# Optimization experiments

Measured on AMD Instinct MI355X. Metric: run time of the kernel, lower is better.

Reference implementation:

```python
import jax, jax.numpy as jnp
import numpy as np

N_CELLS, C_N, K, D_N = 128, 256, 16, 64
G, HS, HM, HMOD, HEADS = 8, 128, 128, 64, 4


def setup_inputs() -> dict:
    key = jax.random.key(0)
    ks = list(jax.random.split(key, 12))
    rng = np.random.default_rng(0)
    # top-K neighbors per neuron within each cell, self excluded, sorted (as in __init__)
    scores = rng.random((N_CELLS, C_N, C_N), dtype=np.float32)
    scores[:, np.arange(C_N), np.arange(C_N)] = -np.inf
    topk = np.argpartition(-scores, K, axis=-1)[..., :K]
    conn_idx = jnp.asarray(np.sort(topk, axis=-1).astype(np.int32))
    cell_to_group = jnp.asarray((np.arange(N_CELLS) % G).astype(np.int32))

    def nrm(k, shape, scale):
        return jax.random.normal(k, shape, dtype=jnp.float32) * scale

    inp = {
        'h': nrm(ks[0], (N_CELLS, C_N, D_N), 1.0),
        'neuron_id': nrm(ks[1], (N_CELLS, C_N, D_N), 0.02),
        'neuron_key': nrm(ks[2], (N_CELLS, C_N, D_N), 0.02),
        'state_w1': nrm(ks[3], (HS, 2 * D_N), (2.0 / (2 * D_N)) ** 0.5),
        'state_b1': jnp.zeros((HS,), jnp.float32),
        'state_gs1': jnp.ones((G, HS), jnp.float32),
        'state_gb1': jnp.zeros((G, HS), jnp.float32),
        'state_w2': nrm(ks[4], (D_N, HS), 0.1 * (2.0 / HS) ** 0.5),
        'state_b2': jnp.zeros((D_N,), jnp.float32),
        'state_gs2': jnp.ones((G, D_N), jnp.float32),
        'state_gb2': jnp.zeros((G, D_N), jnp.float32),
        'msg_w1': nrm(ks[5], (HM, 2 * D_N), (2.0 / (2 * D_N)) ** 0.5),
        'msg_b1': jnp.zeros((HM,), jnp.float32),
        'msg_gs1': jnp.ones((G, HM), jnp.float32),
        'msg_gb1': jnp.zeros((G, HM), jnp.float32),
        'msg_w2': nrm(ks[6], (D_N, HM), 0.1 * (2.0 / HM) ** 0.5),
        'msg_b2': jnp.zeros((D_N,), jnp.float32),
        'msg_gs2': jnp.ones((G, D_N), jnp.float32),
        'msg_gb2': jnp.zeros((G, D_N), jnp.float32),
        'mod_w1': nrm(ks[7], (N_CELLS, D_N, HMOD), (2.0 / D_N) ** 0.5),
        'mod_b1': jnp.zeros((N_CELLS, HMOD), jnp.float32),
        'mod_w2': nrm(ks[8], (N_CELLS, HMOD, D_N), 0.01 * (2.0 / HMOD) ** 0.5),
        'mod_b2': jnp.zeros((N_CELLS, D_N), jnp.float32),
        'conn_idx': conn_idx,
        'cell_to_group': cell_to_group,
    }
    return inp


def reference(h, neuron_id, neuron_key,
              state_w1, state_b1, state_gs1, state_gb1,
              state_w2, state_b2, state_gs2, state_gb2,
              msg_w1, msg_b1, msg_gs1, msg_gb1,
              msg_w2, msg_b2, msg_gs2, msg_gb2,
              mod_w1, mod_b1, mod_w2, mod_b2,
              conn_idx, cell_to_group):
    g = cell_to_group  # [N]
    dh = D_N // HEADS
    gather = jax.vmap(lambda per_cell, idx: per_cell[idx])  # [C,D],[C,K] -> [C,K,D]

    nbr = gather(h, conn_idx)          # [N,C,K,D] neighbor states
    kid = gather(neuron_id, conn_idx)  # [N,C,K,D] neighbor identity vectors

    # multi-head attention weights over the K neighbors
    q = neuron_key.reshape(N_CELLS, C_N, HEADS, dh)
    kk = kid.reshape(N_CELLS, C_N, K, HEADS, dh)
    logits = jnp.einsum('nchd,nckhd->nckh', q, kk) / (dh ** 0.5)
    attn = jax.nn.softmax(logits, axis=2)  # softmax over K

    # per-edge message MLP with per-group gain/bias
    x = jnp.concatenate([nbr, jnp.broadcast_to(h[:, :, None, :], nbr.shape)], axis=-1)  # [N,C,K,2D]
    m1 = jax.nn.gelu(jnp.einsum('nckf,hf->nckh', x, msg_w1) + msg_b1)
    m1 = m1 * msg_gs1[g][:, None, None, :] + msg_gb1[g][:, None, None, :]
    m2 = jnp.einsum('nckh,dh->nckd', m1, msg_w2) + msg_b2
    m2 = m2 * msg_gs2[g][:, None, None, :] + msg_gb2[g][:, None, None, :]

    # attention-weighted aggregation over neighbors
    m2h = m2.reshape(N_CELLS, C_N, K, HEADS, dh)
    agg = jnp.einsum('nckh,nckhd->nchd', attn, m2h).reshape(N_CELLS, C_N, D_N)

    # state-update MLP with per-group gain/bias
    s_in = jnp.concatenate([h, agg], axis=-1)  # [N,C,2D]
    s1 = jax.nn.gelu(jnp.einsum('ncf,hf->nch', s_in, state_w1) + state_b1)
    s1 = s1 * state_gs1[g][:, None, :] + state_gb1[g][:, None, :]
    delta = jnp.einsum('nch,dh->ncd', s1, state_w2) + state_b2
    delta = delta * state_gs2[g][:, None, :] + state_gb2[g][:, None, :]

    # per-cell batched modulation MLP (mod_w1/mod_w2) gating the update
    pooled = h.mean(axis=1)  # [N,D]
    mh = jnp.tanh(jnp.einsum('nd,ndh->nh', pooled, mod_w1) + mod_b1)
    gate = jnp.tanh(jnp.einsum('nh,nho->no', mh, mod_w2) + mod_b2)  # [N,D]

    return h + gate[:, None, :] * delta
```

## Files before the change

### kernel.cpp

```cpp
#include <hip/hip_runtime.h>
#include <hip/hip_bf16.h>

#define N_CELLS 128
#define C_N     256
#define K_NB    16
#define D_N     64
#define G_N     8
#define HS      128
#define HM      128
#define HMOD    64

typedef __bf16 bf16x8 __attribute__((ext_vector_type(8)));
typedef float  f32x4v __attribute__((ext_vector_type(4)));
typedef _Float16 half2_t __attribute__((ext_vector_type(2)));


__device__ __forceinline__ unsigned cvtpk(float lo, float hi) {
    __hip_bfloat162 t = __float22bfloat162_rn(float2{lo, hi});
    return *reinterpret_cast<unsigned*>(&t);
}

__device__ __forceinline__ unsigned short f2bf(float f) {
    return (unsigned short)(cvtpk(f, 0.f) & 0xffffu);
}

__device__ __forceinline__ float bflo(unsigned u) { return __uint_as_float(u << 16); }
__device__ __forceinline__ float bfhi(unsigned u) { return __uint_as_float(u & 0xffff0000u); }

__device__ __forceinline__ half2_t pkrtz(float lo, float hi) {
    return __builtin_bit_cast(half2_t, __builtin_amdgcn_cvt_pkrtz(lo, hi));
}

__device__ __forceinline__ half2_t h2(unsigned u) {
    return __builtin_bit_cast(half2_t, u);
}

__device__ __forceinline__ f32x4v mfma16(uint4 a, uint4 b, f32x4v c) {
    return __builtin_amdgcn_mfma_f32_16x16x32_bf16(
        __builtin_bit_cast(bf16x8, a), __builtin_bit_cast(bf16x8, b), c, 0, 0, 0);
}

__device__ __forceinline__ float gelu_f(float x) {
    float x2 = x * x;
    float u  = x * fmaf(x2, 0.044715f, 1.0f);
    float e  = __expf(1.5957691216057308f * u);
    float r  = __builtin_amdgcn_rcpf(e + 1.0f);
    return x - x * r;
}

__device__ __forceinline__ float sgelu(float x) {
    float e = __expf(-1.702f * x);
    float r = __builtin_amdgcn_rcpf(e + 1.0f);
    return x * r;
}

__device__ __forceinline__ float tanh_fast(float z) {
    float e = __expf(2.0f * z);
    return 1.0f - 2.0f / (e + 1.0f);
}

__device__ __forceinline__ uint4 packf8(const float* p) {
    float4 a = *(const float4*)p, b = *(const float4*)(p + 4);
    return make_uint4(cvtpk(a.x, a.y), cvtpk(a.z, a.w), cvtpk(b.x, b.y), cvtpk(b.z, b.w));
}

__device__ __forceinline__ void load_w2_folded(
    const float* __restrict__ w2, const float* __restrict__ gs1,
    const float* __restrict__ gb1, const float* __restrict__ gs2,
    const float* __restrict__ b2, const float* __restrict__ gb2,
    int g, int lrow, int lgrp, uint4 wf[4][4], float c2[4])
{
    #pragma unroll
    for (int nb2 = 0; nb2 < 4; ++nb2) {
        int d = nb2 * 16 + lrow;
        float gs2d = gs2[g * 64 + d];
        float cgb = 0.0f;
        #pragma unroll
        for (int kf = 0; kf < 4; ++kf) {
            int k0 = kf * 32 + lgrp * 8;
            const float* wp = w2 + d * 128 + k0;
            float4 wa = *(const float4*)wp, wb = *(const float4*)(wp + 4);
            const float* gp = gs1 + g * 128 + k0;
            float4 ga = *(const float4*)gp, gbv = *(const float4*)(gp + 4);
            const float* bp = gb1 + g * 128 + k0;
            float4 ba = *(const float4*)bp, bbv = *(const float4*)(bp + 4);
            cgb += wa.x*ba.x + wa.y*ba.y + wa.z*ba.z + wa.w*ba.w
                 + wb.x*bbv.x + wb.y*bbv.y + wb.z*bbv.z + wb.w*bbv.w;
            wf[nb2][kf] = make_uint4(
                cvtpk(wa.x*ga.x*gs2d,  wa.y*ga.y*gs2d),
                cvtpk(wa.z*ga.z*gs2d,  wa.w*ga.w*gs2d),
                cvtpk(wb.x*gbv.x*gs2d, wb.y*gbv.y*gs2d),
                cvtpk(wb.z*gbv.z*gs2d, wb.w*gbv.w*gs2d));
        }
        cgb += __shfl_xor(cgb, 16);
        cgb += __shfl_xor(cgb, 32);
        c2[nb2] = fmaf(gs2d, cgb + b2[d], gb2[g * 64 + d]);
    }
}


__global__ __launch_bounds__(512, 2) void prep_kernel(
    const float* __restrict__ h, const float* __restrict__ neuron_id,
    const float* __restrict__ neuron_key,
    const float* __restrict__ msg_w1, const float* __restrict__ msg_b1,
    const float* __restrict__ mod_w1, const float* __restrict__ mod_b1,
    const float* __restrict__ mod_w2, const float* __restrict__ mod_b2,
    const int* __restrict__ conn_idx,
    unsigned short* __restrict__ yws, unsigned short* __restrict__ bews,
    unsigned* __restrict__ att2, float* __restrict__ gatep)
{
    __shared__ __align__(16) unsigned short shmem[8][16 * 256];
    int tid = threadIdx.x, bid = blockIdx.x;
    int wave = tid >> 6, lane = tid & 63;
    int lrow = lane & 15, lgrp = lane >> 4;

    if (bid < 256) {
        int n = bid >> 1;
        int c0 = (bid & 1) * 128 + wave * 16;
        unsigned short* ybuf = shmem[wave];

        uint4 bf[2];
        {
            const float* hp = h + ((size_t)n * C_N + (c0 + lrow)) * 64;
            bf[0] = packf8(hp + lgrp * 8);
            bf[1] = packf8(hp + 32 + lgrp * 8);
        }
        for (int nbM = 0; nbM < 16; ++nbM) {
            int o = nbM * 16 + lrow;
            uint4 af[2];
            #pragma unroll
            for (int kf = 0; kf < 2; ++kf) {
                int k = kf * 32 + lgrp * 8;
                const float* wp = (o < 128) ? (msg_w1 + (size_t)o * 128 + k)
                                            : (msg_w1 + (size_t)(o - 128) * 128 + 64 + k);
                af[kf] = packf8(wp);
            }
            f32x4v acc = {0.f, 0.f, 0.f, 0.f};
            acc = mfma16(af[0], bf[0], acc);
            acc = mfma16(af[1], bf[1], acc);
            float4 addv = {0.f, 0.f, 0.f, 0.f};
            if (nbM >= 8) addv = *(const float4*)(msg_b1 + (nbM - 8) * 16 + lgrp * 4);
            uint2 pk = make_uint2(cvtpk(acc[0] + addv.x, acc[1] + addv.y),
                                  cvtpk(acc[2] + addv.z, acc[3] + addv.w));
            int byte = lrow * 512 + ((nbM * 32 + lgrp * 8) ^ ((lrow & 7) << 4));
            *reinterpret_cast<uint2*>(reinterpret_cast<char*>(ybuf) + byte) = pk;
        }
        #pragma unroll
        for (int pass = 0; pass < 8; ++pass) {
            int idx = pass * 64 + lane;
            int row = idx >> 5, col = idx & 31;
            int byte = row * 512 + ((col * 16) ^ ((row & 7) << 4));
            uint4 v = *reinterpret_cast<const uint4*>(
                reinterpret_cast<const char*>(ybuf) + byte);
            size_t rb = (((size_t)n * C_N + c0 + row) * 128) * 2;
            if (col < 16)
                *reinterpret_cast<uint4*>(reinterpret_cast<char*>(yws) + rb + col * 16) = v;
            else
                *reinterpret_cast<uint4*>(reinterpret_cast<char*>(bews) + rb + (col - 16) * 16) = v;
        }
    } else if (bid < 512) {
        int t = lgrp;
        int base = (bid - 256) * 128 + wave * 16;
        for (int i = 0; i < 16; ++i) {
            int gidx = base + i;
            int jv = conn_idx[(size_t)gidx * 16 + lrow];
            const float* kp = neuron_id + ((size_t)(gidx & ~255) + jv) * 64 + t * 16;
            const float* qp = neuron_key + (size_t)gidx * 64 + t * 16;
            float4 k0 = *(const float4*)kp,       k1 = *(const float4*)(kp + 4),
                   k2 = *(const float4*)(kp + 8), k3 = *(const float4*)(kp + 12);
            float4 q0 = *(const float4*)qp,       q1 = *(const float4*)(qp + 4),
                   q2 = *(const float4*)(qp + 8), q3 = *(const float4*)(qp + 12);
            float dt = k0.x*q0.x + k0.y*q0.y + k0.z*q0.z + k0.w*q0.w
                     + k1.x*q1.x + k1.y*q1.y + k1.z*q1.z + k1.w*q1.w
                     + k2.x*q2.x + k2.y*q2.y + k2.z*q2.z + k2.w*q2.w
                     + k3.x*q3.x + k3.y*q3.y + k3.z*q3.z + k3.w*q3.w;
            float lg = dt * 0.25f;
            float mx = lg;
            mx = fmaxf(mx, __shfl_xor(mx, 1));
            mx = fmaxf(mx, __shfl_xor(mx, 2));
            mx = fmaxf(mx, __shfl_xor(mx, 4));
            mx = fmaxf(mx, __shfl_xor(mx, 8));
            float ex = __expf(lg - mx);
            float sm = ex;
            sm += __shfl_xor(sm, 1);
            sm += __shfl_xor(sm, 2);
            sm += __shfl_xor(sm, 4);
            sm += __shfl_xor(sm, 8);
            float av = ex * __builtin_amdgcn_rcpf(sm);
            float avn = __shfl_down(av, 1);
            if ((lrow & 1) == 0) {
                att2[(size_t)gidx * 32 + (lrow >> 1) * 4 + t] =
                    __builtin_bit_cast(unsigned, __builtin_amdgcn_cvt_pkrtz(av, avn));
            }
        }
    } else {
        int n = bid - 512;
        float* red   = reinterpret_cast<float*>(shmem);
        float* pooled = red + 8 * 64;
        float* mh     = pooled + 64;
        int d = lane, part = wave;
        const float* hn = h + (size_t)n * C_N * 64;
        float acc = 0.0f;
        #pragma unroll 4
        for (int i = 0; i < 32; ++i) acc += hn[(part * 32 + i) * 64 + d];
        red[part * 64 + d] = acc;
        __syncthreads();
        if (tid < 64) {
            float s = 0.0f;
            #pragma unroll
            for (int p = 0; p < 8; ++p) s += red[p * 64 + d];
            pooled[d] = s * (1.0f / 256.0f);
        }
        __syncthreads();
        if (tid < 64) {
            float a1 = mod_b1[n * HMOD + d];
            for (int q = 0; q < 64; ++q)
                a1 = fmaf(pooled[q], mod_w1[((size_t)n * 64 + q) * HMOD + d], a1);
            mh[d] = tanh_fast(a1);
        }
        __syncthreads();
        if (tid < 64) {
            float a2 = mod_b2[n * 64 + d];
            for (int q = 0; q < HMOD; ++q)
                a2 = fmaf(mh[q], mod_w2[((size_t)n * HMOD + q) * 64 + d], a2);
            gatep[n * 64 + d] = tanh_fast(a2);
        }
    }
}


__global__ __launch_bounds__(1024, 4) void edge_kernel(
    const unsigned short* __restrict__ yws, const unsigned short* __restrict__ bews,
    const unsigned* __restrict__ att2, const int* __restrict__ conn_idx,
    const float* __restrict__ msg_w2, const float* __restrict__ msg_gs1,
    const float* __restrict__ msg_gb1, const float* __restrict__ msg_gs2,
    const float* __restrict__ msg_b2, const float* __restrict__ msg_gb2,
    const int* __restrict__ cell_to_group,
    unsigned short* __restrict__ aggws)
{
    __shared__ __align__(16) uint4 w2l[16 * 64];
    __shared__ float mb2cl[64];
    __shared__ __align__(16) unsigned short pbuf_all[16][8 * 128];
    __shared__ __align__(16) unsigned short aggT_all[16][2 * 64];
    int tid = threadIdx.x, bid = blockIdx.x;
    int n = bid >> 1;
    int wave = tid >> 6, lane = tid & 63;
    int lrow = lane & 15, lgrp = lane >> 4;
    int base = n * C_N + (bid & 1) * 128 + wave * 8;

    if (wave == 0) {
        uint4 w2f[4][4];
        float mb2c[4];
        int g = cell_to_group[n];
        load_w2_folded(msg_w2, msg_gs1, msg_gb1, msg_gs2, msg_b2, msg_gb2,
                       g, lrow, lgrp, w2f, mb2c);
        #pragma unroll
        for (int t = 0; t < 4; ++t) {
            #pragma unroll
            for (int kf = 0; kf < 4; ++kf)
                w2l[(t * 4 + kf) * 64 + lane] = w2f[t][kf];
            if (lgrp == 0) mb2cl[t * 16 + lrow] = mb2c[t];
        }
    }
    __syncthreads();

    float mb2r0 = mb2cl[lrow], mb2r1 = mb2cl[16 + lrow],
          mb2r2 = mb2cl[32 + lrow], mb2r3 = mb2cl[48 + lrow];
    char* pbuf_b = reinterpret_cast<char*>(pbuf_all[wave]);
    char* aggT_b = reinterpret_cast<char*>(aggT_all[wave]);
    const unsigned* bews32 = (const unsigned*)bews;
    const char* ycell = (const char*)yws + (size_t)n * C_N * 256;

    #pragma unroll 1
    for (int pr = 0; pr < 4; ++pr) {
        int gA = base + pr * 2, gB = gA + 1;
        int jvA = conn_idx[(size_t)gA * 16 + lrow];
        int jvB = conn_idx[(size_t)gB * 16 + lrow];
        unsigned bepA = bews32[(size_t)gA * 64 + lane];
        unsigned bepB = bews32[(size_t)gB * 64 + lane];
        float beA0 = bflo(bepA), beA1 = bfhi(bepA);
        float beB0 = bflo(bepB), beB1 = bfhi(bepB);

        float pA[4][2] = {{0.f,0.f},{0.f,0.f},{0.f,0.f},{0.f,0.f}};
        float pB[4][2] = {{0.f,0.f},{0.f,0.f},{0.f,0.f},{0.f,0.f}};

        #pragma unroll
        for (int kp = 0; kp < 8; ++kp) {
            int jA0 = __builtin_amdgcn_readlane(jvA, 2 * kp);
            int jA1 = __builtin_amdgcn_readlane(jvA, 2 * kp + 1);
            int jB0 = __builtin_amdgcn_readlane(jvB, 2 * kp);
            int jB1 = __builtin_amdgcn_readlane(jvB, 2 * kp + 1);
            unsigned uyA0 = *reinterpret_cast<const unsigned*>(
                ycell + (size_t)jA0 * 256 + lane * 4);
            unsigned uyA1 = *reinterpret_cast<const unsigned*>(
                ycell + (size_t)jA1 * 256 + lane * 4);
            unsigned uyB0 = *reinterpret_cast<const unsigned*>(
                ycell + (size_t)jB0 * 256 + lane * 4);
            unsigned uyB1 = *reinterpret_cast<const unsigned*>(
                ycell + (size_t)jB1 * 256 + lane * 4);
            uint4 aqA = *reinterpret_cast<const uint4*>(att2 + (size_t)gA * 32 + kp * 4);
            uint4 aqB = *reinterpret_cast<const uint4*>(att2 + (size_t)gB * 32 + kp * 4);

            float gA00 = sgelu(bflo(uyA0) + beA0), gA01 = sgelu(bfhi(uyA0) + beA1);
            float gA10 = sgelu(bflo(uyA1) + beA0), gA11 = sgelu(bfhi(uyA1) + beA1);
            float gB00 = sgelu(bflo(uyB0) + beB0), gB01 = sgelu(bfhi(uyB0) + beB1);
            float gB10 = sgelu(bflo(uyB1) + beB0), gB11 = sgelu(bfhi(uyB1) + beB1);
            half2_t GA0 = pkrtz(gA00, gA10);
            half2_t GA1 = pkrtz(gA01, gA11);
            half2_t GB0 = pkrtz(gB00, gB10);
            half2_t GB1 = pkrtz(gB01, gB11);

            half2_t hA, hB;
            hA = h2(aqA.x); hB = h2(aqB.x);
            pA[0][0] = __builtin_amdgcn_fdot2(GA0, hA, pA[0][0], false);
            pA[0][1] = __builtin_amdgcn_fdot2(GA1, hA, pA[0][1], false);
            pB[0][0] = __builtin_amdgcn_fdot2(GB0, hB, pB[0][0], false);
            pB[0][1] = __builtin_amdgcn_fdot2(GB1, hB, pB[0][1], false);
            hA = h2(aqA.y); hB = h2(aqB.y);
            pA[1][0] = __builtin_amdgcn_fdot2(GA0, hA, pA[1][0], false);
            pA[1][1] = __builtin_amdgcn_fdot2(GA1, hA, pA[1][1], false);
            pB[1][0] = __builtin_amdgcn_fdot2(GB0, hB, pB[1][0], false);
            pB[1][1] = __builtin_amdgcn_fdot2(GB1, hB, pB[1][1], false);
            hA = h2(aqA.z); hB = h2(aqB.z);
            pA[2][0] = __builtin_amdgcn_fdot2(GA0, hA, pA[2][0], false);
            pA[2][1] = __builtin_amdgcn_fdot2(GA1, hA, pA[2][1], false);
            pB[2][0] = __builtin_amdgcn_fdot2(GB0, hB, pB[2][0], false);
            pB[2][1] = __builtin_amdgcn_fdot2(GB1, hB, pB[2][1], false);
            hA = h2(aqA.w); hB = h2(aqB.w);
            pA[3][0] = __builtin_amdgcn_fdot2(GA0, hA, pA[3][0], false);
            pA[3][1] = __builtin_amdgcn_fdot2(GA1, hA, pA[3][1], false);
            pB[3][0] = __builtin_amdgcn_fdot2(GB0, hB, pB[3][0], false);
            pB[3][1] = __builtin_amdgcn_fdot2(GB1, hB, pB[3][1], false);
        }

        #pragma unroll
        for (int t = 0; t < 4; ++t) {
            int rowA = t * 2, rowB = rowA + 1;
            *reinterpret_cast<unsigned*>(
                pbuf_b + rowA * 256 + ((lane * 4) ^ ((rowA & 7) << 4))) =
                cvtpk(pA[t][0], pA[t][1]);
            *reinterpret_cast<unsigned*>(
                pbuf_b + rowB * 256 + ((lane * 4) ^ ((rowB & 7) << 4))) =
                cvtpk(pB[t][0], pB[t][1]);
        }

        #pragma unroll
        for (int t = 0; t < 4; ++t) {
            f32x4v acc = {0.f, 0.f, 0.f, 0.f};
            #pragma unroll
            for (int kf = 0; kf < 4; ++kf) {
                int row = t * 2 + (lrow & 1);
                uint4 a = *reinterpret_cast<const uint4*>(
                    pbuf_b + row * 256 + ((kf * 64 + lgrp * 16) ^ ((row & 7) << 4)));
                acc = mfma16(a, w2l[(t * 4 + kf) * 64 + lane], acc);
            }
            if (lgrp == 0) {
                float mb = (t == 0) ? mb2r0 : (t == 1) ? mb2r1 : (t == 2) ? mb2r2 : mb2r3;
                #pragma unroll
                for (int r = 0; r < 2; ++r) {
                    float v = acc[r] + mb;
                    int byte = r * 128 + ((((t * 16 + lrow)) * 2) ^ ((r & 7) << 4));
                    *reinterpret_cast<unsigned short*>(aggT_b + byte) = f2bf(v);
                }
            }
        }
        if (lane < 16) {
            int row = lane >> 3, col = lane & 7;
            int byte = row * 128 + ((col * 16) ^ ((row & 7) << 4));
            uint4 v = *reinterpret_cast<const uint4*>(aggT_b + byte);
            *reinterpret_cast<uint4*>(
                (char*)aggws + (size_t)(gA + row) * 128 + col * 16) = v;
        }
    }
}


__global__ __launch_bounds__(512, 4) void state_kernel(
    const float* __restrict__ h, const unsigned short* __restrict__ aggws,
    const float* __restrict__ gatep,
    const float* __restrict__ state_w1, const float* __restrict__ state_b1,
    const float* __restrict__ state_gs1, const float* __restrict__ state_gb1,
    const float* __restrict__ state_w2, const float* __restrict__ state_b2,
    const float* __restrict__ state_gs2, const float* __restrict__ state_gb2,
    const int* __restrict__ cell_to_group, float* __restrict__ out)
{
    __shared__ __align__(16) unsigned short w1s[128 * 128];
    __shared__ __align__(16) unsigned short s1b_all[8][16 * 128];
    int tid = threadIdx.x, bid = blockIdx.x;
    int n = bid >> 1;
    int g = cell_to_group[n];

    for (int idx = tid; idx < 2048; idx += 512) {
        int row = idx >> 4, ch = idx & 15;
        uint4 p = packf8(state_w1 + (size_t)row * 128 + ch * 8);
        int byte = row * 256 + ((ch * 16) ^ ((row & 7) << 4));
        *reinterpret_cast<uint4*>(reinterpret_cast<char*>(w1s) + byte) = p;
    }
    __syncthreads();

    int wave = tid >> 6, lane = tid & 63;
    int lrow = lane & 15, lgrp = lane >> 4;
    int c0 = (bid & 1) * 128 + wave * 16;
    unsigned short* s1b = s1b_all[wave];

    uint4 sB[4];
    {
        const float* hp = h + ((size_t)n * C_N + c0 + lrow) * 64;
        sB[0] = packf8(hp + lgrp * 8);
        sB[1] = packf8(hp + 32 + lgrp * 8);
        const char* ap = (const char*)aggws + ((size_t)n * C_N + c0 + lrow) * 128;
        sB[2] = *reinterpret_cast<const uint4*>(ap + lgrp * 16);
        sB[3] = *reinterpret_cast<const uint4*>(ap + 64 + lgrp * 16);
    }
    for (int nbM = 0; nbM < 8; ++nbM) {
        uint4 wA[4];
        #pragma unroll
        for (int kf = 0; kf < 4; ++kf)
            wA[kf] = *reinterpret_cast<const uint4*>(
                reinterpret_cast<const char*>(w1s) +
                (nbM * 16 + lrow) * 256 + ((kf * 64 + lgrp * 16) ^ ((lrow & 7) << 4)));
        f32x4v acc = {0.f, 0.f, 0.f, 0.f};
        #pragma unroll
        for (int kf = 0; kf < 4; ++kf) acc = mfma16(wA[kf], sB[kf], acc);
        float4 b1q = *(const float4*)(state_b1 + nbM * 16 + lgrp * 4);
        float g0 = gelu_f(acc[0] + b1q.x), g1 = gelu_f(acc[1] + b1q.y);
        float g2 = gelu_f(acc[2] + b1q.z), g3 = gelu_f(acc[3] + b1q.w);
        uint2 pk = make_uint2(cvtpk(g0, g1), cvtpk(g2, g3));
        int byte = lrow * 256 + ((nbM * 32 + lgrp * 8) ^ ((lrow & 7) << 4));
        *reinterpret_cast<uint2*>(reinterpret_cast<char*>(s1b) + byte) = pk;
    }

    uint4 w2sf[4][4];
    float sb2c[4];
    load_w2_folded(state_w2, state_gs1, state_gb1, state_gs2, state_b2, state_gb2,
                   g, lrow, lgrp, w2sf, sb2c);
    uint4 s1A[4];
    #pragma unroll
    for (int kf = 0; kf < 4; ++kf)
        s1A[kf] = *reinterpret_cast<const uint4*>(
            reinterpret_cast<const char*>(s1b) +
            lrow * 256 + ((kf * 64 + lgrp * 16) ^ ((lrow & 7) << 4)));

    float* dT = reinterpret_cast<float*>(s1b);
    #pragma unroll
    for (int nb2 = 0; nb2 < 4; ++nb2) {
        f32x4v acc = {0.f, 0.f, 0.f, 0.f};
        #pragma unroll
        for (int kf = 0; kf < 4; ++kf) acc = mfma16(s1A[kf], w2sf[nb2][kf], acc);
        #pragma unroll
        for (int r = 0; r < 4; ++r) {
            int c = lgrp * 4 + r;
            int d = nb2 * 16 + lrow;
            int byte = c * 256 + ((d * 4) ^ ((c & 7) << 4));
            *reinterpret_cast<float*>(reinterpret_cast<char*>(dT) + byte) = acc[r] + sb2c[nb2];
        }
    }
    #pragma unroll
    for (int pass = 0; pass < 4; ++pass) {
        int idx = pass * 64 + lane;
        int row = idx >> 4, col = idx & 15;
        int byte = row * 256 + ((col * 16) ^ ((row & 7) << 4));
        float4 dv = *reinterpret_cast<const float4*>(reinterpret_cast<const char*>(dT) + byte);
        size_t off = ((size_t)n * C_N + c0 + row) * 64 + col * 4;
        float4 hv = *(const float4*)(h + off);
        float4 gv = *(const float4*)(gatep + n * 64 + col * 4);
        float4 o;
        o.x = fmaf(gv.x, dv.x, hv.x);
        o.y = fmaf(gv.y, dv.y, hv.y);
        o.z = fmaf(gv.z, dv.z, hv.z);
        o.w = fmaf(gv.w, dv.w, hv.w);
        *(float4*)(out + off) = o;
    }
}


extern "C" void kernel_launch(void* const* d_in, const int* in_sizes, int n_in,
                              void* d_out, int out_size, void* d_ws, size_t ws_size,
                              hipStream_t stream) {
    (void)in_sizes; (void)n_in; (void)out_size; (void)ws_size;
    const float* h          = (const float*)d_in[0];
    const float* neuron_id  = (const float*)d_in[1];
    const float* neuron_key = (const float*)d_in[2];
    const float* state_w1   = (const float*)d_in[3];
    const float* state_b1   = (const float*)d_in[4];
    const float* state_gs1  = (const float*)d_in[5];
    const float* state_gb1  = (const float*)d_in[6];
    const float* state_w2   = (const float*)d_in[7];
    const float* state_b2   = (const float*)d_in[8];
    const float* state_gs2  = (const float*)d_in[9];
    const float* state_gb2  = (const float*)d_in[10];
    const float* msg_w1     = (const float*)d_in[11];
    const float* msg_b1     = (const float*)d_in[12];
    const float* msg_gs1    = (const float*)d_in[13];
    const float* msg_gb1    = (const float*)d_in[14];
    const float* msg_w2     = (const float*)d_in[15];
    const float* msg_b2     = (const float*)d_in[16];
    const float* msg_gs2    = (const float*)d_in[17];
    const float* msg_gb2    = (const float*)d_in[18];
    const float* mod_w1     = (const float*)d_in[19];
    const float* mod_b1     = (const float*)d_in[20];
    const float* mod_w2     = (const float*)d_in[21];
    const float* mod_b2     = (const float*)d_in[22];
    const int*   conn_idx   = (const int*)d_in[23];
    const int*   c2g        = (const int*)d_in[24];

    char* ws = (char*)d_ws;
    float*          gatep = (float*)ws;
    unsigned short* yws   = (unsigned short*)(ws + (32u << 10));
    unsigned short* bews  = (unsigned short*)(ws + (32u << 10) + (8u << 20));
    unsigned*       att2  = (unsigned*)(ws + (32u << 10) + (16u << 20));
    unsigned short* aggws = (unsigned short*)(ws + (32u << 10) + (24u << 20));
    float* outp = (float*)d_out;

    prep_kernel<<<dim3(640), dim3(512), 0, stream>>>(
        h, neuron_id, neuron_key, msg_w1, msg_b1,
        mod_w1, mod_b1, mod_w2, mod_b2, conn_idx,
        yws, bews, att2, gatep);
    edge_kernel<<<dim3(256), dim3(1024), 0, stream>>>(
        yws, bews, att2, conn_idx,
        msg_w2, msg_gs1, msg_gb1, msg_gs2, msg_b2, msg_gb2, c2g, aggws);
    state_kernel<<<dim3(256), dim3(512), 0, stream>>>(
        h, aggws, gatep,
        state_w1, state_b1, state_gs1, state_gb1,
        state_w2, state_b2, state_gs2, state_gb2, c2g, outp);
}
```

Measured before the change: 110.1 us.

## Precompute folded msg_w2 per group in prep and shrink edge blocks

Adds an extra prep block that computes the group-folded msg_w2 fragments and bias for all 8 groups once and stores them to workspace, so edge blocks just copy them into LDS instead of each recomputing the fold. The edge kernel is reshaped from 256 blocks of 1024 threads to 2048 blocks of 256 threads, each handling 16 neurons, with an interleaved block-to-cell mapping. This gives more, smaller blocks for better occupancy and load balance across CUs, at the cost of more redundant per-block LDS weight loads.

Measured after the change: 145.0 us. 31.7% more time.

```diff
diff --git a/kernel.cpp b/kernel.cpp
--- a/kernel.cpp
+++ b/kernel.cpp
@@ -103,11 +103,15 @@
     const float* __restrict__ h, const float* __restrict__ neuron_id,
     const float* __restrict__ neuron_key,
     const float* __restrict__ msg_w1, const float* __restrict__ msg_b1,
+    const float* __restrict__ msg_w2, const float* __restrict__ msg_gs1,
+    const float* __restrict__ msg_gb1, const float* __restrict__ msg_gs2,
+    const float* __restrict__ msg_b2, const float* __restrict__ msg_gb2,
     const float* __restrict__ mod_w1, const float* __restrict__ mod_b1,
     const float* __restrict__ mod_w2, const float* __restrict__ mod_b2,
     const int* __restrict__ conn_idx,
     unsigned short* __restrict__ yws, unsigned short* __restrict__ bews,
-    unsigned* __restrict__ att2, float* __restrict__ gatep)
+    unsigned* __restrict__ att2, float* __restrict__ gatep,
+    uint4* __restrict__ wsfold, float* __restrict__ mb2ws)
 {
     __shared__ __align__(16) unsigned short shmem[8][16 * 256];
     int tid = threadIdx.x, bid = blockIdx.x;
@@ -193,7 +197,7 @@
                     __builtin_bit_cast(unsigned, __builtin_amdgcn_cvt_pkrtz(av, avn));
             }
         }
-    } else {
+    } else if (bid < 640) {
         int n = bid - 512;
         float* red   = reinterpret_cast<float*>(shmem);
         float* pooled = red + 8 * 64;
@@ -225,42 +229,48 @@
                 a2 = fmaf(mh[q], mod_w2[((size_t)n * HMOD + q) * 64 + d], a2);
             gatep[n * 64 + d] = tanh_fast(a2);
         }
-    }
-}
-
-
-__global__ __launch_bounds__(1024, 4) void edge_kernel(
+    } else {
+        int g = wave;
+        uint4 wf[4][4];
+        float c2[4];
+        load_w2_folded(msg_w2, msg_gs1, msg_gb1, msg_gs2, msg_b2, msg_gb2,
+                       g, lrow, lgrp, wf, c2);
+        #pragma unroll
+        for (int t = 0; t < 4; ++t) {
+            #pragma unroll
+            for (int kf = 0; kf < 4; ++kf)
+                wsfold[((size_t)g * 16 + t * 4 + kf) * 64 + lane] = wf[t][kf];
+            if (lgrp == 0) mb2ws[g * 64 + t * 16 + lrow] = c2[t];
+        }
+    }
+}
+
+
+__global__ __launch_bounds__(256, 5) void edge_kernel(
     const unsigned short* __restrict__ yws, const unsigned short* __restrict__ bews,
     const unsigned* __restrict__ att2, const int* __restrict__ conn_idx,
-    const float* __restrict__ msg_w2, const float* __restrict__ msg_gs1,
-    const float* __restrict__ msg_gb1, const float* __restrict__ msg_gs2,
-    const float* __restrict__ msg_b2, const float* __restrict__ msg_gb2,
+    const uint4* __restrict__ wsfold, const float* __restrict__ mb2ws,
     const int* __restrict__ cell_to_group,
     unsigned short* __restrict__ aggws)
 {
     __shared__ __align__(16) uint4 w2l[16 * 64];
     __shared__ float mb2cl[64];
-    __shared__ __align__(16) unsigned short pbuf_all[16][8 * 128];
-    __shared__ __align__(16) unsigned short aggT_all[16][2 * 64];
+    __shared__ __align__(16) unsigned short pbuf_all[4][8 * 128];
+    __shared__ __align__(16) unsigned short aggT_all[4][2 * 64];
     int tid = threadIdx.x, bid = blockIdx.x;
-    int n = bid >> 1;
+    int w = ((bid & 7) << 8) | (bid >> 3);
+    int n = w >> 4;
+    int sec = w & 15;
     int wave = tid >> 6, lane = tid & 63;
     int lrow = lane & 15, lgrp = lane >> 4;
-    int base = n * C_N + (bid & 1) * 128 + wave * 8;
-
-    if (wave == 0) {
-        uint4 w2f[4][4];
-        float mb2c[4];
+    int base = n * C_N + sec * 16 + wave * 4;
+
+    {
         int g = cell_to_group[n];
-        load_w2_folded(msg_w2, msg_gs1, msg_gb1, msg_gs2, msg_b2, msg_gb2,
-                       g, lrow, lgrp, w2f, mb2c);
-        #pragma unroll
-        for (int t = 0; t < 4; ++t) {
-            #pragma unroll
-            for (int kf = 0; kf < 4; ++kf)
-                w2l[(t * 4 + kf) * 64 + lane] = w2f[t][kf];
-            if (lgrp == 0) mb2cl[t * 16 + lrow] = mb2c[t];
-        }
+        const uint4* wsrc = wsfold + (size_t)g * 16 * 64;
+        #pragma unroll
+        for (int i = 0; i < 4; ++i) w2l[i * 256 + tid] = wsrc[i * 256 + tid];
+        if (tid < 64) mb2cl[tid] = mb2ws[g * 64 + tid];
     }
     __syncthreads();
 
@@ -272,7 +282,7 @@
     const char* ycell = (const char*)yws + (size_t)n * C_N * 256;
 
     #pragma unroll 1
-    for (int pr = 0; pr < 4; ++pr) {
+    for (int pr = 0; pr < 2; ++pr) {
         int gA = base + pr * 2, gB = gA + 1;
         int jvA = conn_idx[(size_t)gA * 16 + lrow];
         int jvB = conn_idx[(size_t)gB * 16 + lrow];
@@ -510,15 +520,17 @@
     unsigned short* bews  = (unsigned short*)(ws + (32u << 10) + (8u << 20));
     unsigned*       att2  = (unsigned*)(ws + (32u << 10) + (16u << 20));
     unsigned short* aggws = (unsigned short*)(ws + (32u << 10) + (24u << 20));
+    uint4*          wsfold = (uint4*)(ws + (32u << 10) + (28u << 20));
+    float*          mb2ws  = (float*)(ws + (32u << 10) + (28u << 20) + (128u << 10));
     float* outp = (float*)d_out;
 
-    prep_kernel<<<dim3(640), dim3(512), 0, stream>>>(
+    prep_kernel<<<dim3(641), dim3(512), 0, stream>>>(
         h, neuron_id, neuron_key, msg_w1, msg_b1,
+        msg_w2, msg_gs1, msg_gb1, msg_gs2, msg_b2, msg_gb2,
         mod_w1, mod_b1, mod_w2, mod_b2, conn_idx,
-        yws, bews, att2, gatep);
-    edge_kernel<<<dim3(256), dim3(1024), 0, stream>>>(
-        yws, bews, att2, conn_idx,
-        msg_w2, msg_gs1, msg_gb1, msg_gs2, msg_b2, msg_gb2, c2g, aggws);
+        yws, bews, att2, gatep, wsfold, mb2ws);
+    edge_kernel<<<dim3(2048), dim3(256), 0, stream>>>(
+        yws, bews, att2, conn_idx, wsfold, mb2ws, c2g, aggws);
     state_kernel<<<dim3(256), dim3(512), 0, stream>>>(
         h, aggws, gatep,
         state_w1, state_b1, state_gs1, state_gb1,
```
